# Kernel tuning notes

Hardware: AMD Instinct MI355X
Metric: run time of the kernel (lower is better)

The kernel has to match this reference:

```python
import jax, jax.numpy as jnp
import numpy as np

MAX_SCALE_MUL = float(np.log(100.0))
EPS = 1e-12

def _l2norm(t):
    # F.normalize(dim=-1): x / max(||x||_2, eps)
    n = jnp.sqrt(jnp.sum(t * t, axis=-1, keepdims=True))
    return t / jnp.maximum(n, EPS)

def setup_inputs() -> dict:
    key = jax.random.key(0)
    ks = jax.random.split(key, 6)
    B, L, C, H = 2, 2048, 1024, 16
    x = jax.random.normal(ks[0], (B, L, C), dtype=jnp.float32)
    attn_bias = jax.random.normal(ks[1], (1, 1, L, L), dtype=jnp.float32) * 0.02
    W_qkv = jax.random.normal(ks[2], (3 * C, C), dtype=jnp.float32) * (1.0 / np.sqrt(C))
    q_bias = jnp.zeros((C,), dtype=jnp.float32)
    v_bias = jnp.zeros((C,), dtype=jnp.float32)
    scale_mul_1H11 = jnp.full((1, H, 1, 1), np.log(4.0), dtype=jnp.float32)
    W_proj = jax.random.normal(ks[3], (C, C), dtype=jnp.float32) * (1.0 / np.sqrt(C))
    b_proj = jnp.zeros((C,), dtype=jnp.float32)
    return {"x": x, "attn_bias": attn_bias, "W_qkv": W_qkv, "q_bias": q_bias,
            "v_bias": v_bias, "scale_mul_1H11": scale_mul_1H11,
            "W_proj": W_proj, "b_proj": b_proj}

def reference(x, attn_bias, W_qkv, q_bias, v_bias, scale_mul_1H11, W_proj, b_proj):
    B, L, C = x.shape
    H = scale_mul_1H11.shape[1]
    D = C // H
    # qkv projection (no linear bias) + concatenated (q_bias, 0, v_bias)
    bias = jnp.concatenate([q_bias, jnp.zeros_like(q_bias), v_bias])
    pre_qkv = jnp.einsum('blc,oc->blo', x, W_qkv) + bias  # (B,L,3C)
    qkv = pre_qkv.reshape(B, L, 3, H, D).transpose(2, 0, 3, 1, 4)  # (3,B,H,L,D)
    q, k, v = qkv[0], qkv[1], qkv[2]
    # cosine attention: l2-normalize q,k; q scaled by learned per-head scale
    scale_mul = jnp.exp(jnp.minimum(scale_mul_1H11, MAX_SCALE_MUL))
    q = _l2norm(q) * scale_mul
    k = _l2norm(k)
    # slow_attn_original with scale=1 (attn_l2_norm path)
    attn = jnp.einsum('bhld,bhmd->bhlm', q, k) + attn_bias  # (B,H,L,L)
    attn = jax.nn.softmax(attn, axis=-1)
    oup = jnp.einsum('bhlm,bhmd->bhld', attn, v)  # (B,H,L,D)
    oup = oup.transpose(0, 2, 1, 3).reshape(B, L, C)
    return jnp.einsum('blc,oc->blo', oup, W_proj) + b_proj
```

## Files before the change

kernel.cpp:

```cpp
#include <hip/hip_runtime.h>

typedef short bf16x8 __attribute__((ext_vector_type(8)));
typedef unsigned short u16x8 __attribute__((ext_vector_type(8)));
typedef float f32x4 __attribute__((ext_vector_type(4)));
typedef float f32x16 __attribute__((ext_vector_type(16)));
typedef unsigned int u32x2 __attribute__((ext_vector_type(2)));

#define LOG2E 1.44269504088896340736f

__device__ __forceinline__ float bf2f(unsigned short u) {
  union { unsigned int i; float f; } v; v.i = ((unsigned int)u) << 16; return v.f;
}
__device__ __forceinline__ unsigned short f2bf(float f) {
  union { float fl; unsigned int i; } v; v.fl = f;
  unsigned int r = v.i + 0x7FFFu + ((v.i >> 16) & 1u);
  return (unsigned short)(r >> 16);
}
__device__ __forceinline__ unsigned int cvt_pk_bf16(float lo, float hi) {
  unsigned int d;
  asm("v_cvt_pk_bf16_f32 %0, %1, %2" : "=v"(d) : "v"(lo), "v"(hi));
  return d;
}
__device__ __forceinline__ void perm_swap(unsigned int& a, unsigned int& b) {
  asm("v_permlane32_swap_b32 %0, %1" : "+v"(a), "+v"(b));
}
__device__ __forceinline__ bf16x8 mk8(unsigned int a, unsigned int b,
                                      unsigned int c, unsigned int d) {
  union { unsigned int u[4]; bf16x8 v; } r;
  r.u[0] = a; r.u[1] = b; r.u[2] = c; r.u[3] = d;
  return r.v;
}
__device__ __forceinline__ void gload_lds16(const void* g, void* l) {
  __builtin_amdgcn_global_load_lds(
      (const __attribute__((address_space(1))) void*)g,
      (__attribute__((address_space(3))) void*)l, 16, 0, 0);
}

__global__ __launch_bounds__(256) void cvt_all(const float* __restrict__ x,
                                               const float* __restrict__ wqkv,
                                               const float* __restrict__ wproj,
                                               unsigned short* __restrict__ xb,
                                               unsigned short* __restrict__ wqb,
                                               unsigned short* __restrict__ wpb) {
  int i = blockIdx.x * 256 + threadIdx.x;
  const float* src; unsigned short* dst; int off;
  if (i < 524288)       { src = x;     dst = xb;  off = i; }
  else if (i < 917504)  { src = wqkv;  dst = wqb; off = i - 524288; }
  else                  { src = wproj; dst = wpb; off = i - 917504; }
  float4 a = ((const float4*)src)[2 * off];
  float4 b = ((const float4*)src)[2 * off + 1];
  u16x8 o;
  o[0] = f2bf(a.x); o[1] = f2bf(a.y); o[2] = f2bf(a.z); o[3] = f2bf(a.w);
  o[4] = f2bf(b.x); o[5] = f2bf(b.y); o[6] = f2bf(b.z); o[7] = f2bf(b.w);
  ((u16x8*)dst)[off] = o;
}

__global__ __launch_bounds__(256) void prep_bias(const float* __restrict__ bias,
                                                 unsigned short* __restrict__ biasArr) {
  int tid = blockIdx.x * 256 + threadIdx.x;
  int kg = tid & 1;
  int l = (tid >> 1) & 63;
  int w = (tid >> 7) & 3;
  int kb = (tid >> 9) & 31;
  int qt = (tid >> 14) & 15;
  int q = qt * 128 + w * 32 + (l & 31);
  int kbase = kb * 64 + kg * 32 + (l >> 5) * 4;
  const float* src = bias + (size_t)q * 2048 + kbase;
  u16x8 oa, ob;
#pragma unroll
  for (int rr = 0; rr < 4; ++rr) {
    float4 g = *(const float4*)(src + rr * 8);
    unsigned short e0 = f2bf(g.x * LOG2E), e1 = f2bf(g.y * LOG2E);
    unsigned short e2 = f2bf(g.z * LOG2E), e3 = f2bf(g.w * LOG2E);
    if (rr < 2) {
      oa[rr * 4 + 0] = e0; oa[rr * 4 + 1] = e1; oa[rr * 4 + 2] = e2; oa[rr * 4 + 3] = e3;
    } else {
      ob[(rr - 2) * 4 + 0] = e0; ob[(rr - 2) * 4 + 1] = e1;
      ob[(rr - 2) * 4 + 2] = e2; ob[(rr - 2) * 4 + 3] = e3;
    }
  }
  int base = (((qt * 32 + kb) * 4 + w) * 4 + kg * 2) * 64 + l;
  ((u16x8*)biasArr)[base] = oa;
  ((u16x8*)biasArr)[base + 64] = ob;
}

template <bool F32OUT>
__global__ __launch_bounds__(256) void gemm_nt(const unsigned short* __restrict__ A,
                                               const unsigned short* __restrict__ B,
                                               void* __restrict__ Cout,
                                               const float* __restrict__ bias,
                                               int M, int N, int K) {
  __shared__ __align__(16) unsigned short a_lds[128 * 64];
  __shared__ __align__(16) unsigned short b_lds[128 * 64];
  const int t = threadIdx.x;
  const int lane = t & 63, w = t >> 6;
  const int wm = w >> 1, wn = w & 1;
  const int r16 = lane >> 4, c16 = lane & 15;
  const int m0 = blockIdx.y * 128, n0 = blockIdx.x * 128;
  f32x4 acc[4][4] = {};
  for (int k0 = 0; k0 < K; k0 += 64) {
#pragma unroll
    for (int i = 0; i < 4; ++i) {
      int s = i * 256 + t;
      int row = s >> 3, c = s & 7;
      int cs = c ^ (row & 7);
      gload_lds16(A + (size_t)(m0 + row) * K + k0 + cs * 8, (char*)a_lds + s * 16);
      gload_lds16(B + (size_t)(n0 + row) * K + k0 + cs * 8, (char*)b_lds + s * 16);
    }
    __syncthreads();
#pragma unroll
    for (int ks = 0; ks < 2; ++ks) {
      bf16x8 af[4], bfr[4];
#pragma unroll
      for (int mi = 0; mi < 4; ++mi) {
        int row = wm * 64 + mi * 16 + c16;
        int ch = (r16 + ks * 4) ^ (row & 7);
        af[mi] = *(const bf16x8*)&a_lds[row * 64 + ch * 8];
      }
#pragma unroll
      for (int ni = 0; ni < 4; ++ni) {
        int row = wn * 64 + ni * 16 + c16;
        int ch = (r16 + ks * 4) ^ (row & 7);
        bfr[ni] = *(const bf16x8*)&b_lds[row * 64 + ch * 8];
      }
#pragma unroll
      for (int mi = 0; mi < 4; ++mi)
#pragma unroll
        for (int ni = 0; ni < 4; ++ni)
          acc[mi][ni] = __builtin_amdgcn_mfma_f32_16x16x32_bf16(af[mi], bfr[ni], acc[mi][ni], 0, 0, 0);
    }
    __syncthreads();
  }
#pragma unroll
  for (int mi = 0; mi < 4; ++mi)
#pragma unroll
    for (int ni = 0; ni < 4; ++ni)
#pragma unroll
      for (int r = 0; r < 4; ++r) {
        int m = m0 + wm * 64 + mi * 16 + r16 * 4 + r;
        int n = n0 + wn * 64 + ni * 16 + c16;
        float v = acc[mi][ni][r];
        if constexpr (F32OUT) {
          ((float*)Cout)[(size_t)m * N + n] = v + bias[n];
        } else {
          ((unsigned short*)Cout)[(size_t)m * N + n] = f2bf(v);
        }
      }
}

template <bool F32OUT>
__global__ __launch_bounds__(256) void gemm_nt64(const unsigned short* __restrict__ A,
                                                 const unsigned short* __restrict__ B,
                                                 void* __restrict__ Cout,
                                                 const float* __restrict__ bias,
                                                 int M, int N, int K) {
  __shared__ __align__(16) unsigned short a_lds[128 * 64];
  __shared__ __align__(16) unsigned short b_lds[64 * 64];
  const int t = threadIdx.x;
  const int lane = t & 63, w = t >> 6;
  const int wm = w >> 1, wn = w & 1;
  const int r16 = lane >> 4, c16 = lane & 15;
  const int m0 = blockIdx.y * 128, n0 = blockIdx.x * 64;
  f32x4 acc[4][2] = {};
  for (int k0 = 0; k0 < K; k0 += 64) {
#pragma unroll
    for (int i = 0; i < 4; ++i) {
      int s = i * 256 + t;
      int row = s >> 3, c = s & 7;
      int cs = c ^ (row & 7);
      gload_lds16(A + (size_t)(m0 + row) * K + k0 + cs * 8, (char*)a_lds + s * 16);
    }
#pragma unroll
    for (int i = 0; i < 2; ++i) {
      int s = i * 256 + t;
      int row = s >> 3, c = s & 7;
      int cs = c ^ (row & 7);
      gload_lds16(B + (size_t)(n0 + row) * K + k0 + cs * 8, (char*)b_lds + s * 16);
    }
    __syncthreads();
#pragma unroll
    for (int ks = 0; ks < 2; ++ks) {
      bf16x8 af[4], bfr[2];
#pragma unroll
      for (int mi = 0; mi < 4; ++mi) {
        int row = wm * 64 + mi * 16 + c16;
        int ch = (r16 + ks * 4) ^ (row & 7);
        af[mi] = *(const bf16x8*)&a_lds[row * 64 + ch * 8];
      }
#pragma unroll
      for (int ni = 0; ni < 2; ++ni) {
        int row = wn * 32 + ni * 16 + c16;
        int ch = (r16 + ks * 4) ^ (row & 7);
        bfr[ni] = *(const bf16x8*)&b_lds[row * 64 + ch * 8];
      }
#pragma unroll
      for (int mi = 0; mi < 4; ++mi)
#pragma unroll
        for (int ni = 0; ni < 2; ++ni)
          acc[mi][ni] = __builtin_amdgcn_mfma_f32_16x16x32_bf16(af[mi], bfr[ni], acc[mi][ni], 0, 0, 0);
    }
    __syncthreads();
  }
#pragma unroll
  for (int mi = 0; mi < 4; ++mi)
#pragma unroll
    for (int ni = 0; ni < 2; ++ni)
#pragma unroll
      for (int r = 0; r < 4; ++r) {
        int m = m0 + wm * 64 + mi * 16 + r16 * 4 + r;
        int n = n0 + wn * 32 + ni * 16 + c16;
        float v = acc[mi][ni][r];
        if constexpr (F32OUT) {
          ((float*)Cout)[(size_t)m * N + n] = v + bias[n];
        } else {
          ((unsigned short*)Cout)[(size_t)m * N + n] = f2bf(v);
        }
      }
}

__global__ __launch_bounds__(256) void norm_pack(const unsigned short* __restrict__ pre,
                                                 const float* __restrict__ q_bias,
                                                 const float* __restrict__ v_bias,
                                                 const float* __restrict__ scale_mul,
                                                 unsigned short* __restrict__ qo,
                                                 unsigned short* __restrict__ ko,
                                                 unsigned short* __restrict__ vto) {
  __shared__ float tl[64][65];
  const int t = threadIdx.x;
  const int li = t >> 2, dq = t & 3;
  const int tile = blockIdx.x;
  const int sl = blockIdx.y;
  const int qkv = sl >> 4, h = sl & 15;
  const int b = tile >> 5, lt = tile & 31;
  const int l = lt * 64 + li;
  const int dbase = dq * 16;
  const unsigned short* src = pre + ((size_t)b * 2048 + l) * 3072 + qkv * 1024 + h * 64 + dbase;
  float v[16];
  bf16x8 x0 = *(const bf16x8*)src;
  bf16x8 x1 = *(const bf16x8*)(src + 8);
#pragma unroll
  for (int j = 0; j < 8; ++j) {
    v[j] = bf2f((unsigned short)x0[j]);
    v[8 + j] = bf2f((unsigned short)x1[j]);
  }
  if (qkv == 0) {
#pragma unroll
    for (int j = 0; j < 16; ++j) v[j] += q_bias[h * 64 + dbase + j];
  } else if (qkv == 2) {
#pragma unroll
    for (int j = 0; j < 16; ++j) v[j] += v_bias[h * 64 + dbase + j];
  }
  if (qkv < 2) {
    float ss = 0.f;
#pragma unroll
    for (int j = 0; j < 16; ++j) ss += v[j] * v[j];
    ss += __shfl_xor(ss, 1);
    ss += __shfl_xor(ss, 2);
    float inv = 1.0f / fmaxf(sqrtf(ss), 1e-12f);
    if (qkv == 0) inv *= __expf(fminf(scale_mul[h], 4.6051701859880914f));
    u16x8 o0, o1;
#pragma unroll
    for (int j = 0; j < 8; ++j) {
      o0[j] = f2bf(v[j] * inv);
      o1[j] = f2bf(v[8 + j] * inv);
    }
    unsigned short* dst = (qkv == 0 ? qo : ko) + ((size_t)(b * 16 + h) * 2048 + l) * 64 + dbase;
    *(u16x8*)dst = o0;
    *(u16x8*)(dst + 8) = o1;
  } else {
#pragma unroll
    for (int j = 0; j < 16; ++j) tl[li][dbase + j] = v[j];
    __syncthreads();
    const int d = li;
    const int lb = dq * 16;
    u16x8 o0, o1;
#pragma unroll
    for (int j = 0; j < 8; ++j) {
      o0[j] = f2bf(tl[lb + j][d]);
      o1[j] = f2bf(tl[lb + 8 + j][d]);
    }
    unsigned short* dst = vto + ((size_t)(b * 16 + h) * 64 + d) * 2048 + lt * 64 + lb;
    *(u16x8*)dst = o0;
    *(u16x8*)(dst + 8) = o1;
  }
}

__global__ __launch_bounds__(256) void attn_fwd(const unsigned short* __restrict__ qb,
                                                const unsigned short* __restrict__ kbuf,
                                                const unsigned short* __restrict__ vtb,
                                                const unsigned short* __restrict__ biasArr,
                                                unsigned short* __restrict__ oup) {
  __shared__ __align__(16) unsigned short k_lds[2][4096];
  __shared__ __align__(16) unsigned short vt_lds[2][4096];
  __shared__ __align__(16) unsigned short b_lds[2][8192];
  const int t = threadIdx.x;
  const int lane = t & 63, w = t >> 6;
  const int l31 = lane & 31, hi = lane >> 5;
  const int bid = blockIdx.x;
  const int swz = (bid & 7) * 64 + (bid >> 3);
  const int bh = swz >> 4;
  const int qt = swz & 15;
  const int q0 = qt * 128;
  const int h = bh & 15;
  const size_t base = (size_t)bh * 2048 * 64;
  const unsigned short* kp = kbuf + base + (size_t)(t & 31) * 64 +
                             ((t >> 6) & 3) * 16 + ((t >> 5) & 1) * 8;
  const unsigned short* vp = vtb + base + (size_t)(t & 31) * 2048 +
                             ((t >> 6) & 3) * 16 + ((t >> 5) & 1) * 8;
  const unsigned short* bsrc = biasArr + (size_t)qt * 262144 + t * 8;
  bf16x8 qf[4];
  {
    const unsigned short* qp = qb + base + (size_t)(q0 + w * 32 + l31) * 64 + hi * 8;
    qf[0] = *(const bf16x8*)qp;
    qf[1] = *(const bf16x8*)(qp + 16);
    qf[2] = *(const bf16x8*)(qp + 32);
    qf[3] = *(const bf16x8*)(qp + 48);
  }
  f32x16 o0 = {}, o1 = {};
  float ls0 = 0.f, ls1 = 0.f;

  gload_lds16(kp, (char*)k_lds[0] + t * 16);
  gload_lds16(kp + 2048, (char*)k_lds[0] + t * 16 + 4096);
  gload_lds16(vp, (char*)vt_lds[0] + t * 16);
  gload_lds16(vp + 32 * 2048, (char*)vt_lds[0] + t * 16 + 4096);
#pragma unroll
  for (int i = 0; i < 4; ++i)
    gload_lds16(bsrc + i * 2048, (char*)b_lds[0] + t * 16 + i * 4096);

  for (int kb = 0; kb < 32; ++kb) {
    const int cur = kb & 1;
    __syncthreads();
    if (kb + 1 < 32) {
      const int nxt = cur ^ 1;
      gload_lds16(kp + (size_t)(kb + 1) * 4096, (char*)k_lds[nxt] + t * 16);
      gload_lds16(kp + (size_t)(kb + 1) * 4096 + 2048, (char*)k_lds[nxt] + t * 16 + 4096);
      gload_lds16(vp + (kb + 1) * 64, (char*)vt_lds[nxt] + t * 16);
      gload_lds16(vp + (kb + 1) * 64 + 32 * 2048, (char*)vt_lds[nxt] + t * 16 + 4096);
#pragma unroll
      for (int i = 0; i < 4; ++i)
        gload_lds16(bsrc + (kb + 1) * 8192 + i * 2048, (char*)b_lds[nxt] + t * 16 + i * 4096);
    }
    f32x16 s0 = {}, s1 = {};
    __builtin_amdgcn_s_setprio(1);
#pragma unroll
    for (int dc = 0; dc < 4; ++dc) {
      bf16x8 kf0 = *(const bf16x8*)&k_lds[cur][dc * 512 + lane * 8];
      bf16x8 kf1 = *(const bf16x8*)&k_lds[cur][(4 + dc) * 512 + lane * 8];
      s0 = __builtin_amdgcn_mfma_f32_32x32x16_bf16(kf0, qf[dc], s0, 0, 0, 0);
      s1 = __builtin_amdgcn_mfma_f32_32x32x16_bf16(kf1, qf[dc], s1, 0, 0, 0);
    }
    __builtin_amdgcn_s_setprio(0);
    const unsigned short* bl = b_lds[cur] + w * 2048 + lane * 8;
    bf16x8 b0 = *(const bf16x8*)(bl);
    bf16x8 b1 = *(const bf16x8*)(bl + 512);
    bf16x8 b2 = *(const bf16x8*)(bl + 1024);
    bf16x8 b3 = *(const bf16x8*)(bl + 1536);
    float p0[16], p1[16];
#pragma unroll
    for (int r = 0; r < 8; ++r) {
      p0[r] = __builtin_amdgcn_exp2f(__builtin_fmaf(s0[r], LOG2E, bf2f((unsigned short)b0[r])));
      p0[8 + r] = __builtin_amdgcn_exp2f(__builtin_fmaf(s0[8 + r], LOG2E, bf2f((unsigned short)b1[r])));
      p1[r] = __builtin_amdgcn_exp2f(__builtin_fmaf(s1[r], LOG2E, bf2f((unsigned short)b2[r])));
      p1[8 + r] = __builtin_amdgcn_exp2f(__builtin_fmaf(s1[8 + r], LOG2E, bf2f((unsigned short)b3[r])));
    }
#pragma unroll
    for (int r = 0; r < 16; ++r) { ls0 += p0[r]; ls1 += p1[r]; }
    unsigned int x0 = cvt_pk_bf16(p0[0], p0[1]), x1 = cvt_pk_bf16(p0[2], p0[3]);
    unsigned int y0 = cvt_pk_bf16(p0[4], p0[5]), y1 = cvt_pk_bf16(p0[6], p0[7]);
    unsigned int z0 = cvt_pk_bf16(p0[8], p0[9]), z1 = cvt_pk_bf16(p0[10], p0[11]);
    unsigned int w0 = cvt_pk_bf16(p0[12], p0[13]), w1 = cvt_pk_bf16(p0[14], p0[15]);
    perm_swap(x0, y0); perm_swap(x1, y1); perm_swap(z0, w0); perm_swap(z1, w1);
    bf16x8 pf0 = mk8(x0, x1, y0, y1);
    bf16x8 pf1 = mk8(z0, z1, w0, w1);
    unsigned int a0 = cvt_pk_bf16(p1[0], p1[1]), a1 = cvt_pk_bf16(p1[2], p1[3]);
    unsigned int c0 = cvt_pk_bf16(p1[4], p1[5]), c1 = cvt_pk_bf16(p1[6], p1[7]);
    unsigned int d0 = cvt_pk_bf16(p1[8], p1[9]), d1 = cvt_pk_bf16(p1[10], p1[11]);
    unsigned int e0 = cvt_pk_bf16(p1[12], p1[13]), e1 = cvt_pk_bf16(p1[14], p1[15]);
    perm_swap(a0, c0); perm_swap(a1, c1); perm_swap(d0, e0); perm_swap(d1, e1);
    bf16x8 pf2 = mk8(a0, a1, c0, c1);
    bf16x8 pf3 = mk8(d0, d1, e0, e1);
    bf16x8 pf[4] = {pf0, pf1, pf2, pf3};
    __builtin_amdgcn_s_setprio(1);
#pragma unroll
    for (int kc = 0; kc < 4; ++kc) {
      bf16x8 vf0 = *(const bf16x8*)&vt_lds[cur][kc * 512 + lane * 8];
      bf16x8 vf1 = *(const bf16x8*)&vt_lds[cur][(4 + kc) * 512 + lane * 8];
      o0 = __builtin_amdgcn_mfma_f32_32x32x16_bf16(vf0, pf[kc], o0, 0, 0, 0);
      o1 = __builtin_amdgcn_mfma_f32_32x32x16_bf16(vf1, pf[kc], o1, 0, 0, 0);
    }
    __builtin_amdgcn_s_setprio(0);
  }
  float lsum = ls0 + ls1;
  lsum += __shfl_xor(lsum, 32);
  float inv = 1.0f / lsum;
  const int b = bh >> 4;
  unsigned short* orow = oup + ((size_t)b * 2048 + q0 + w * 32 + l31) * 1024 + h * 64;
#pragma unroll
  for (int dg = 0; dg < 2; ++dg) {
#pragma unroll
    for (int rr = 0; rr < 4; ++rr) {
      float v0 = (dg ? o1[rr * 4 + 0] : o0[rr * 4 + 0]) * inv;
      float v1 = (dg ? o1[rr * 4 + 1] : o0[rr * 4 + 1]) * inv;
      float v2 = (dg ? o1[rr * 4 + 2] : o0[rr * 4 + 2]) * inv;
      float v3 = (dg ? o1[rr * 4 + 3] : o0[rr * 4 + 3]) * inv;
      u32x2 pk2;
      pk2[0] = cvt_pk_bf16(v0, v1);
      pk2[1] = cvt_pk_bf16(v2, v3);
      int d = dg * 32 + rr * 8 + hi * 4;
      *(u32x2*)(orow + d) = pk2;
    }
  }
}

extern "C" void kernel_launch(void* const* d_in, const int* in_sizes, int n_in,
                              void* d_out, int out_size, void* d_ws, size_t ws_size,
                              hipStream_t stream) {
  const float* x = (const float*)d_in[0];
  const float* attn_bias = (const float*)d_in[1];
  const float* W_qkv = (const float*)d_in[2];
  const float* q_bias = (const float*)d_in[3];
  const float* v_bias = (const float*)d_in[4];
  const float* scale_mul = (const float*)d_in[5];
  const float* W_proj = (const float*)d_in[6];
  const float* b_proj = (const float*)d_in[7];
  float* out = (float*)d_out;
  char* ws = (char*)d_ws;

  unsigned short* x_bf = (unsigned short*)(ws + 0);
  unsigned short* wqkv_bf = (unsigned short*)(ws + 8388608);
  unsigned short* wproj_bf = (unsigned short*)(ws + 14680064);
  unsigned short* biasArr = (unsigned short*)(ws + 16777216);
  unsigned short* q_pk = (unsigned short*)(ws + 25165824);
  unsigned short* k_pk = (unsigned short*)(ws + 33554432);
  unsigned short* vt_pk = (unsigned short*)(ws + 41943040);
  unsigned short* oup_bf = (unsigned short*)(ws + 50331648);
  unsigned short* pre_qkv = (unsigned short*)(ws + 58720256);

  cvt_all<<<4096, 256, 0, stream>>>(x, W_qkv, W_proj, x_bf, wqkv_bf, wproj_bf);
  prep_bias<<<1024, 256, 0, stream>>>(attn_bias, biasArr);
  gemm_nt<false><<<dim3(24, 32), 256, 0, stream>>>(x_bf, wqkv_bf, (void*)pre_qkv, nullptr,
                                                   4096, 3072, 1024);
  norm_pack<<<dim3(64, 48), 256, 0, stream>>>(pre_qkv, q_bias, v_bias, scale_mul,
                                              q_pk, k_pk, vt_pk);
  attn_fwd<<<512, 256, 0, stream>>>(q_pk, k_pk, vt_pk, biasArr, oup_bf);
  gemm_nt64<true><<<dim3(16, 32), 256, 0, stream>>>(oup_bf, wproj_bf, (void*)out, b_proj,
                                                    4096, 1024, 1024);
}
```

Measured before the change: 152.5 us.

## Split attention KV range across two wave groups and merge partial outputs in LDS

New measurement: 135.4 us. 1.13x faster.

```diff
diff --git a/kernel.cpp b/kernel.cpp
--- a/kernel.cpp
+++ b/kernel.cpp
@@ -285,16 +285,19 @@
   }
 }
 
-__global__ __launch_bounds__(256) void attn_fwd(const unsigned short* __restrict__ qb,
-                                                const unsigned short* __restrict__ kbuf,
-                                                const unsigned short* __restrict__ vtb,
-                                                const unsigned short* __restrict__ biasArr,
-                                                unsigned short* __restrict__ oup) {
+__global__ __launch_bounds__(512, 4) void attn_fwd(const unsigned short* __restrict__ qb,
+                                                   const unsigned short* __restrict__ kbuf,
+                                                   const unsigned short* __restrict__ vtb,
+                                                   const unsigned short* __restrict__ biasArr,
+                                                   unsigned short* __restrict__ oup) {
   __shared__ __align__(16) unsigned short k_lds[2][4096];
   __shared__ __align__(16) unsigned short vt_lds[2][4096];
   __shared__ __align__(16) unsigned short b_lds[2][8192];
   const int t = threadIdx.x;
   const int lane = t & 63, w = t >> 6;
+  const int sp = w >> 2;
+  const int wq = w & 3;
+  const int tt = t & 255;
   const int l31 = lane & 31, hi = lane >> 5;
   const int bid = blockIdx.x;
   const int swz = (bid & 7) * 64 + (bid >> 3);
@@ -303,111 +306,110 @@
   const int q0 = qt * 128;
   const int h = bh & 15;
   const size_t base = (size_t)bh * 2048 * 64;
-  const unsigned short* kp = kbuf + base + (size_t)(t & 31) * 64 +
-                             ((t >> 6) & 3) * 16 + ((t >> 5) & 1) * 8;
-  const unsigned short* vp = vtb + base + (size_t)(t & 31) * 2048 +
-                             ((t >> 6) & 3) * 16 + ((t >> 5) & 1) * 8;
-  const unsigned short* bsrc = biasArr + (size_t)qt * 262144 + t * 8;
+  const unsigned short* kp = kbuf + base + (size_t)(tt & 31) * 64 +
+                             ((tt >> 6) & 3) * 16 + ((tt >> 5) & 1) * 8;
+  const unsigned short* vp = vtb + base + (size_t)(tt & 31) * 2048 +
+                             ((tt >> 6) & 3) * 16 + ((tt >> 5) & 1) * 8;
+  const unsigned short* bsrc = biasArr + (size_t)qt * 262144 + tt * 8;
   bf16x8 qf[4];
   {
-    const unsigned short* qp = qb + base + (size_t)(q0 + w * 32 + l31) * 64 + hi * 8;
+    const unsigned short* qp = qb + base + (size_t)(q0 + wq * 32 + l31) * 64 + hi * 8;
     qf[0] = *(const bf16x8*)qp;
     qf[1] = *(const bf16x8*)(qp + 16);
     qf[2] = *(const bf16x8*)(qp + 32);
     qf[3] = *(const bf16x8*)(qp + 48);
   }
   f32x16 o0 = {}, o1 = {};
-  float ls0 = 0.f, ls1 = 0.f;
-
-  gload_lds16(kp, (char*)k_lds[0] + t * 16);
-  gload_lds16(kp + 2048, (char*)k_lds[0] + t * 16 + 4096);
-  gload_lds16(vp, (char*)vt_lds[0] + t * 16);
-  gload_lds16(vp + 32 * 2048, (char*)vt_lds[0] + t * 16 + 4096);
-#pragma unroll
-  for (int i = 0; i < 4; ++i)
-    gload_lds16(bsrc + i * 2048, (char*)b_lds[0] + t * 16 + i * 4096);
-
-  for (int kb = 0; kb < 32; ++kb) {
-    const int cur = kb & 1;
-    __syncthreads();
-    if (kb + 1 < 32) {
-      const int nxt = cur ^ 1;
-      gload_lds16(kp + (size_t)(kb + 1) * 4096, (char*)k_lds[nxt] + t * 16);
-      gload_lds16(kp + (size_t)(kb + 1) * 4096 + 2048, (char*)k_lds[nxt] + t * 16 + 4096);
-      gload_lds16(vp + (kb + 1) * 64, (char*)vt_lds[nxt] + t * 16);
-      gload_lds16(vp + (kb + 1) * 64 + 32 * 2048, (char*)vt_lds[nxt] + t * 16 + 4096);
-#pragma unroll
-      for (int i = 0; i < 4; ++i)
-        gload_lds16(bsrc + (kb + 1) * 8192 + i * 2048, (char*)b_lds[nxt] + t * 16 + i * 4096);
-    }
-    f32x16 s0 = {}, s1 = {};
-    __builtin_amdgcn_s_setprio(1);
-#pragma unroll
-    for (int dc = 0; dc < 4; ++dc) {
-      bf16x8 kf0 = *(const bf16x8*)&k_lds[cur][dc * 512 + lane * 8];
-      bf16x8 kf1 = *(const bf16x8*)&k_lds[cur][(4 + dc) * 512 + lane * 8];
-      s0 = __builtin_amdgcn_mfma_f32_32x32x16_bf16(kf0, qf[dc], s0, 0, 0, 0);
-      s1 = __builtin_amdgcn_mfma_f32_32x32x16_bf16(kf1, qf[dc], s1, 0, 0, 0);
-    }
-    __builtin_amdgcn_s_setprio(0);
-    const unsigned short* bl = b_lds[cur] + w * 2048 + lane * 8;
-    bf16x8 b0 = *(const bf16x8*)(bl);
-    bf16x8 b1 = *(const bf16x8*)(bl + 512);
-    bf16x8 b2 = *(const bf16x8*)(bl + 1024);
-    bf16x8 b3 = *(const bf16x8*)(bl + 1536);
-    float p0[16], p1[16];
-#pragma unroll
-    for (int r = 0; r < 8; ++r) {
-      p0[r] = __builtin_amdgcn_exp2f(__builtin_fmaf(s0[r], LOG2E, bf2f((unsigned short)b0[r])));
-      p0[8 + r] = __builtin_amdgcn_exp2f(__builtin_fmaf(s0[8 + r], LOG2E, bf2f((unsigned short)b1[r])));
-      p1[r] = __builtin_amdgcn_exp2f(__builtin_fmaf(s1[r], LOG2E, bf2f((unsigned short)b2[r])));
-      p1[8 + r] = __builtin_amdgcn_exp2f(__builtin_fmaf(s1[8 + r], LOG2E, bf2f((unsigned short)b3[r])));
-    }
-#pragma unroll
-    for (int r = 0; r < 16; ++r) { ls0 += p0[r]; ls1 += p1[r]; }
-    unsigned int x0 = cvt_pk_bf16(p0[0], p0[1]), x1 = cvt_pk_bf16(p0[2], p0[3]);
-    unsigned int y0 = cvt_pk_bf16(p0[4], p0[5]), y1 = cvt_pk_bf16(p0[6], p0[7]);
-    unsigned int z0 = cvt_pk_bf16(p0[8], p0[9]), z1 = cvt_pk_bf16(p0[10], p0[11]);
-    unsigned int w0 = cvt_pk_bf16(p0[12], p0[13]), w1 = cvt_pk_bf16(p0[14], p0[15]);
-    perm_swap(x0, y0); perm_swap(x1, y1); perm_swap(z0, w0); perm_swap(z1, w1);
-    bf16x8 pf0 = mk8(x0, x1, y0, y1);
-    bf16x8 pf1 = mk8(z0, z1, w0, w1);
-    unsigned int a0 = cvt_pk_bf16(p1[0], p1[1]), a1 = cvt_pk_bf16(p1[2], p1[3]);
-    unsigned int c0 = cvt_pk_bf16(p1[4], p1[5]), c1 = cvt_pk_bf16(p1[6], p1[7]);
-    unsigned int d0 = cvt_pk_bf16(p1[8], p1[9]), d1 = cvt_pk_bf16(p1[10], p1[11]);
-    unsigned int e0 = cvt_pk_bf16(p1[12], p1[13]), e1 = cvt_pk_bf16(p1[14], p1[15]);
-    perm_swap(a0, c0); perm_swap(a1, c1); perm_swap(d0, e0); perm_swap(d1, e1);
-    bf16x8 pf2 = mk8(a0, a1, c0, c1);
-    bf16x8 pf3 = mk8(d0, d1, e0, e1);
-    bf16x8 pf[4] = {pf0, pf1, pf2, pf3};
-    __builtin_amdgcn_s_setprio(1);
-#pragma unroll
-    for (int kc = 0; kc < 4; ++kc) {
-      bf16x8 vf0 = *(const bf16x8*)&vt_lds[cur][kc * 512 + lane * 8];
-      bf16x8 vf1 = *(const bf16x8*)&vt_lds[cur][(4 + kc) * 512 + lane * 8];
-      o0 = __builtin_amdgcn_mfma_f32_32x32x16_bf16(vf0, pf[kc], o0, 0, 0, 0);
-      o1 = __builtin_amdgcn_mfma_f32_32x32x16_bf16(vf1, pf[kc], o1, 0, 0, 0);
-    }
-    __builtin_amdgcn_s_setprio(0);
-  }
-  float lsum = ls0 + ls1;
-  lsum += __shfl_xor(lsum, 32);
-  float inv = 1.0f / lsum;
-  const int b = bh >> 4;
-  unsigned short* orow = oup + ((size_t)b * 2048 + q0 + w * 32 + l31) * 1024 + h * 64;
-#pragma unroll
-  for (int dg = 0; dg < 2; ++dg) {
-#pragma unroll
-    for (int rr = 0; rr < 4; ++rr) {
-      float v0 = (dg ? o1[rr * 4 + 0] : o0[rr * 4 + 0]) * inv;
-      float v1 = (dg ? o1[rr * 4 + 1] : o0[rr * 4 + 1]) * inv;
-      float v2 = (dg ? o1[rr * 4 + 2] : o0[rr * 4 + 2]) * inv;
-      float v3 = (dg ? o1[rr * 4 + 3] : o0[rr * 4 + 3]) * inv;
-      u32x2 pk2;
-      pk2[0] = cvt_pk_bf16(v0, v1);
-      pk2[1] = cvt_pk_bf16(v2, v3);
-      int d = dg * 32 + rr * 8 + hi * 4;
-      *(u32x2*)(orow + d) = pk2;
+  float ls = 0.f;
+
+  for (int kbl = 0; kbl < 16; ++kbl) {
+    const int kb = sp * 16 + kbl;
+    gload_lds16(kp + (size_t)kb * 4096, (char*)k_lds[sp] + tt * 16);
+    gload_lds16(kp + (size_t)kb * 4096 + 2048, (char*)k_lds[sp] + tt * 16 + 4096);
+    gload_lds16(vp + kb * 64, (char*)vt_lds[sp] + tt * 16);
+    gload_lds16(vp + kb * 64 + 32 * 2048, (char*)vt_lds[sp] + tt * 16 + 4096);
+#pragma unroll
+    for (int i = 0; i < 4; ++i)
+      gload_lds16(bsrc + kb * 8192 + i * 2048, (char*)b_lds[sp] + tt * 16 + i * 4096);
+    __syncthreads();
+    const unsigned short* bl = b_lds[sp] + wq * 2048 + lane * 8;
+#pragma unroll
+    for (int kg = 0; kg < 2; ++kg) {
+      f32x16 s = {};
+      __builtin_amdgcn_s_setprio(1);
+#pragma unroll
+      for (int dc = 0; dc < 4; ++dc) {
+        bf16x8 kf = *(const bf16x8*)&k_lds[sp][(kg * 4 + dc) * 512 + lane * 8];
+        s = __builtin_amdgcn_mfma_f32_32x32x16_bf16(kf, qf[dc], s, 0, 0, 0);
+      }
+      __builtin_amdgcn_s_setprio(0);
+      bf16x8 b0 = *(const bf16x8*)(bl + kg * 1024);
+      bf16x8 b1 = *(const bf16x8*)(bl + kg * 1024 + 512);
+      float p[16];
+#pragma unroll
+      for (int r = 0; r < 8; ++r) {
+        p[r] = __builtin_amdgcn_exp2f(__builtin_fmaf(s[r], LOG2E, bf2f((unsigned short)b0[r])));
+        p[8 + r] = __builtin_amdgcn_exp2f(__builtin_fmaf(s[8 + r], LOG2E, bf2f((unsigned short)b1[r])));
+      }
+#pragma unroll
+      for (int r = 0; r < 16; ++r) ls += p[r];
+      unsigned int x0 = cvt_pk_bf16(p[0], p[1]), x1 = cvt_pk_bf16(p[2], p[3]);
+      unsigned int y0 = cvt_pk_bf16(p[4], p[5]), y1 = cvt_pk_bf16(p[6], p[7]);
+      unsigned int z0 = cvt_pk_bf16(p[8], p[9]), z1 = cvt_pk_bf16(p[10], p[11]);
+      unsigned int w0 = cvt_pk_bf16(p[12], p[13]), w1 = cvt_pk_bf16(p[14], p[15]);
+      perm_swap(x0, y0); perm_swap(x1, y1); perm_swap(z0, w0); perm_swap(z1, w1);
+      bf16x8 pfa = mk8(x0, x1, y0, y1);
+      bf16x8 pfb = mk8(z0, z1, w0, w1);
+      __builtin_amdgcn_s_setprio(1);
+#pragma unroll
+      for (int kc = 0; kc < 2; ++kc) {
+        bf16x8 pfx = kc ? pfb : pfa;
+        bf16x8 vf0 = *(const bf16x8*)&vt_lds[sp][(kg * 2 + kc) * 512 + lane * 8];
+        bf16x8 vf1 = *(const bf16x8*)&vt_lds[sp][(4 + kg * 2 + kc) * 512 + lane * 8];
+        o0 = __builtin_amdgcn_mfma_f32_32x32x16_bf16(vf0, pfx, o0, 0, 0, 0);
+        o1 = __builtin_amdgcn_mfma_f32_32x32x16_bf16(vf1, pfx, o1, 0, 0, 0);
+      }
+      __builtin_amdgcn_s_setprio(0);
+    }
+    __syncthreads();
+  }
+  float* fO = (float*)b_lds;
+  float* fL = (float*)k_lds;
+  const int slot = wq * 64 + lane;
+  if (sp == 1) {
+#pragma unroll
+    for (int i = 0; i < 16; ++i) {
+      fO[i * 256 + slot] = o0[i];
+      fO[(16 + i) * 256 + slot] = o1[i];
+    }
+    fL[slot] = ls;
+  }
+  __syncthreads();
+  if (sp == 0) {
+#pragma unroll
+    for (int i = 0; i < 16; ++i) {
+      o0[i] += fO[i * 256 + slot];
+      o1[i] += fO[(16 + i) * 256 + slot];
+    }
+    ls += fL[slot];
+    float lsum = ls + __shfl_xor(ls, 32);
+    float inv = 1.0f / lsum;
+    const int b = bh >> 4;
+    unsigned short* orow = oup + ((size_t)b * 2048 + q0 + wq * 32 + l31) * 1024 + h * 64;
+#pragma unroll
+    for (int dg = 0; dg < 2; ++dg) {
+#pragma unroll
+      for (int rr = 0; rr < 4; ++rr) {
+        float v0 = (dg ? o1[rr * 4 + 0] : o0[rr * 4 + 0]) * inv;
+        float v1 = (dg ? o1[rr * 4 + 1] : o0[rr * 4 + 1]) * inv;
+        float v2 = (dg ? o1[rr * 4 + 2] : o0[rr * 4 + 2]) * inv;
+        float v3 = (dg ? o1[rr * 4 + 3] : o0[rr * 4 + 3]) * inv;
+        u32x2 pk2;
+        pk2[0] = cvt_pk_bf16(v0, v1);
+        pk2[1] = cvt_pk_bf16(v2, v3);
+        int d = dg * 32 + rr * 8 + hi * 4;
+        *(u32x2*)(orow + d) = pk2;
+      }
     }
   }
 }
@@ -442,7 +444,7 @@
                                                    4096, 3072, 1024);
   norm_pack<<<dim3(64, 48), 256, 0, stream>>>(pre_qkv, q_bias, v_bias, scale_mul,
                                               q_pk, k_pk, vt_pk);
-  attn_fwd<<<512, 256, 0, stream>>>(q_pk, k_pk, vt_pk, biasArr, oup_bf);
+  attn_fwd<<<512, 512, 0, stream>>>(q_pk, k_pk, vt_pk, biasArr, oup_bf);
   gemm_nt64<true><<<dim3(16, 32), 256, 0, stream>>>(oup_bf, wproj_bf, (void*)out, b_proj,
                                                     4096, 1024, 1024);
 }
```
